# Kernel tuning notes

Hardware: AMD Instinct MI355X
Metric: run time of the kernel (lower is better)

## Reference

```python
import jax, jax.numpy as jnp
import numpy as np

N = 50000   # nodes
E = 400000  # edges (before self-loops)
F = 128     # num_features
H = 8       # heads (layer 1)
C = 64      # hidden_channels
B = 64      # graphs in batch
K = 10      # num_classes
NEG_SLOPE = 0.2


def setup_inputs() -> dict:
    key = jax.random.key(0)
    ks = jax.random.split(key, 12)
    g = lambda k, shape, fan: jax.random.normal(k, shape, jnp.float32) / np.sqrt(fan).astype(np.float32)
    return {
        "x": jax.random.normal(ks[0], (N, F), jnp.float32),
        "edge_index": jax.random.randint(ks[1], (2, E), 0, N, jnp.int32),
        "batch": jnp.sort(jax.random.randint(ks[2], (N,), 0, B, jnp.int32)),
        "W1": g(ks[3], (F, H * C), F),
        "att_src1": g(ks[4], (H, C), C),
        "att_dst1": g(ks[5], (H, C), C),
        "b1": jnp.zeros((H * C,), jnp.float32),
        "W2": g(ks[6], (H * C, C), H * C),
        "att_src2": g(ks[7], (1, C), C),
        "att_dst2": g(ks[8], (1, C), C),
        "b2": jnp.zeros((C,), jnp.float32),
        "lin1_w": g(ks[9], (C, C), C),
        "lin1_b": jnp.zeros((C,), jnp.float32),
        "lin2_w": g(ks[10], (C, K), C),
        "lin2_b": jnp.zeros((K,), jnp.float32),
    }


def gat_conv(x, src, dst, W, att_src, att_dst, bias):
    """PyG GATConv (self-loops already appended to src/dst). x:[N,Fin] -> [N,H*C]."""
    heads, out_c = att_src.shape
    h = (x @ W).reshape(N, heads, out_c)                      # [N,H,C]
    a_s = jnp.einsum('nhc,hc->nh', h, att_src)                # [N,H]
    a_d = jnp.einsum('nhc,hc->nh', h, att_dst)
    e = jax.nn.leaky_relu(a_s[src] + a_d[dst], NEG_SLOPE)     # [E',H]
    # segment softmax over incoming edges of each destination node
    m = jax.ops.segment_max(e, dst, num_segments=N)
    e = jnp.exp(e - m[dst])
    denom = jax.ops.segment_sum(e, dst, num_segments=N)
    alpha = e / (denom[dst] + 1e-16)                          # [E',H]
    out = jax.ops.segment_sum(h[src] * alpha[:, :, None], dst, num_segments=N)  # [N,H,C]
    return out.reshape(N, heads * out_c) + bias


def reference(x, edge_index, batch, W1, att_src1, att_dst1, b1,
              W2, att_src2, att_dst2, b2, lin1_w, lin1_b, lin2_w, lin2_b):
    loops = jnp.arange(N, dtype=edge_index.dtype)
    src = jnp.concatenate([edge_index[0], loops])
    dst = jnp.concatenate([edge_index[1], loops])

    h = gat_conv(x, src, dst, W1, att_src1, att_dst1, b1)     # [N, H*C]
    h = jax.nn.elu(h)                                         # dropout inactive (eval)
    h = gat_conv(h, src, dst, W2, att_src2, att_dst2, b2)     # [N, C]
    h = jax.nn.elu(h)

    pooled = jax.ops.segment_sum(h, batch, num_segments=B)    # global_add_pool -> [B, C]
    z = jax.nn.elu(pooled @ lin1_w + lin1_b)
    logits = z @ lin2_w + lin2_b
    return jax.nn.log_softmax(logits, axis=-1)
```

## Files before the change

kernel.cpp:

```cpp
#include <hip/hip_runtime.h>
#include <hip/hip_bf16.h>

#define DEV static __device__ __forceinline__

constexpr int F1 = 128;
constexpr int H1 = 8;
constexpr int C  = 64;
constexpr int B  = 64;
constexpr int K  = 10;
constexpr float NEG = 0.2f;
constexpr unsigned SMASK = 0x07FFFFFFu;

typedef __attribute__((ext_vector_type(8))) short short8;
typedef __attribute__((ext_vector_type(4))) float floatx4;

DEV float b2f(__hip_bfloat16 x) { return __bfloat162float(x); }
DEV float elu1(float v) { return v > 0.f ? v : (__expf(v) - 1.f); }
DEV unsigned short f2bbits(float f) {
  __hip_bfloat16 b = __float2bfloat16(f);
  return *(unsigned short*)&b;
}
DEV float blo(unsigned u) { return __uint_as_float(u << 16); }
DEV float bhi(unsigned u) { return __uint_as_float(u & 0xffff0000u); }
DEV float bu(unsigned short u) { return __uint_as_float(((unsigned)u) << 16); }
DEV unsigned pack2(float lo, float hi) {
  return (unsigned)f2bbits(lo) | ((unsigned)f2bbits(hi) << 16);
}
DEV float rcp_nr(float x) {
  float r = __builtin_amdgcn_rcpf(x);
  return r * (2.f - x * r);
}


DEV int detect_dev(const void* xraw, int* lds) {
  if (threadIdx.x == 0) {
    const __hip_bfloat16* xb = (const __hip_bfloat16*)xraw;
    int bad = 0;
    for (int i = 0; i < 128; ++i) {
      float v = b2f(xb[2 * i]);
      if (!(fabsf(v) < 1e4f)) bad++;
    }
    *lds = (bad < 13) ? 1 : 0;
  }
  __syncthreads();
  return *lds;
}

#define CVT(p, i) (isbf ? b2f(((const __hip_bfloat16*)(p))[i]) : ((const float*)(p))[i])

__global__ void fused_prep_kernel(const void* x_raw, const void* w1raw,
                                  const void* as1r, const void* ad1r, const void* b1r,
                                  const void* w2raw,
                                  const void* as2r, const void* ad2r, const void* b2r,
                                  const void* l1wr, const void* l1br,
                                  const void* l2wr, const void* l2br,
                                  unsigned short* __restrict__ xbf,
                                  unsigned short* __restrict__ w1frag,
                                  unsigned short* __restrict__ w2frag,
                                  unsigned short* __restrict__ vfrag,
                                  float* __restrict__ wts,
                                  int* __restrict__ deg,
                                  float* __restrict__ pooled,
                                  int nX, int N) {
  __shared__ int fl;
  int isbf = detect_dev(x_raw, &fl);
  int gid = blockIdx.x * 256 + threadIdx.x;
  int stride = gridDim.x * 256;

  int ng = nX >> 3;
  if (isbf) {
    const uint4* src = (const uint4*)x_raw;
    uint4* dst = (uint4*)xbf;
    for (int i = gid; i < ng; i += stride) dst[i] = src[i];
  } else {
    const float4* src = (const float4*)x_raw;
    uint4* dst = (uint4*)xbf;
    for (int i = gid; i < ng; i += stride) {
      float4 a = src[2 * i], b = src[2 * i + 1];
      uint4 o;
      o.x = pack2(a.x, a.y); o.y = pack2(a.z, a.w);
      o.z = pack2(b.x, b.y); o.w = pack2(b.z, b.w);
      dst[i] = o;
    }
  }
  for (int i = ng * 8 + gid; i < nX; i += stride)
    xbf[i] = isbf ? ((const unsigned short*)x_raw)[i]
                  : f2bbits(((const float*)x_raw)[i]);

  for (int i = gid; i < 512;  i += stride) {
    int hp = i >> 7, l16 = (i >> 3) & 15, nt = i & 7;
    int c = hp * 128 + nt * 16 + l16;
    wts[1024 + i] = CVT(b1r, c);
  }
  for (int i = gid; i < 64;   i += stride) wts[1536 + i] = CVT(as2r, i);
  for (int i = gid; i < 64;   i += stride) wts[1600 + i] = CVT(ad2r, i);
  for (int i = gid; i < 64;   i += stride) wts[1664 + i] = CVT(b2r, i);
  for (int i = gid; i < 4096; i += stride) wts[1728 + i] = CVT(l1wr, i);
  for (int i = gid; i < 64;   i += stride) wts[5824 + i] = CVT(l1br, i);
  for (int i = gid; i < 640;  i += stride) wts[5888 + i] = CVT(l2wr, i);
  for (int i = gid; i < 10;   i += stride) wts[6528 + i] = CVT(l2br, i);
  for (int t = gid; t < 8192; t += stride) {
    int lane = t & 63, ks = (t >> 6) & 3, nt = t >> 8;
    for (int j = 0; j < 8; ++j) {
      int k = ks * 32 + (lane >> 4) * 8 + j;
      int n = nt * 16 + (lane & 15);
      w1frag[t * 8 + j] = f2bbits(CVT(w1raw, k * 512 + n));
    }
  }
  for (int t = gid; t < 4096; t += stride) {
    int lane = t & 63, nt = (t >> 6) & 3, ks = t >> 8;
    for (int j = 0; j < 8; ++j) {
      int p = ks * 32 + (lane >> 4) * 8 + j;
      int hp = p >> 7, pl16 = (p >> 3) & 15, pnt = p & 7;
      int k = hp * 128 + pnt * 16 + pl16;
      int n = nt * 16 + (lane & 15);
      w2frag[t * 8 + j] = f2bbits(CVT(w2raw, k * 64 + n));
    }
  }
  for (int t = gid; t < 2048; t += stride) {
    int j = t & 7, lane = (t >> 3) & 63, ks = t >> 9;
    int k = ks * 32 + (lane >> 4) * 8 + j;
    int n = lane & 15;
    int hh = (n < 8) ? n : (n - 8);
    float s = 0.f;
    if (n < 8) {
      for (int c = 0; c < 64; ++c)
        s += CVT(w1raw, k * 512 + hh * 64 + c) * CVT(as1r, hh * 64 + c);
    } else {
      for (int c = 0; c < 64; ++c)
        s += CVT(w1raw, k * 512 + hh * 64 + c) * CVT(ad1r, hh * 64 + c);
    }
    vfrag[(ks * 64 + lane) * 8 + j] = f2bbits(s);
  }
  for (int i = gid; i < N; i += stride) deg[i] = 0;
  for (int i = gid; i < B * C; i += stride) pooled[i] = 0.f;
}

__global__ __launch_bounds__(256) void deg_att_kernel(
    const int* __restrict__ ei, int E, int Etot, int* __restrict__ deg,
    const unsigned short* __restrict__ xbf,
    const unsigned short* __restrict__ vfrag,
    float* __restrict__ a_s, float* __restrict__ a_d,
    int N, int attBlocks) {
  if ((int)blockIdx.x >= attBlocks) {
    int e = ((int)blockIdx.x - attBlocks) * 256 + threadIdx.x;
    if (e < Etot) {
      int d = (e < E) ? ei[E + e] : e - E;
      atomicAdd(&deg[d], 1);
    }
    return;
  }
  int t = threadIdx.x, w = t >> 6, lane = t & 63;
  int quad = lane >> 4, l16 = lane & 15;
  int row0 = blockIdx.x * 64 + w * 16;

  floatx4 acc = {};
  int rl = row0 + l16; if (rl >= N) rl = N - 1;
  const unsigned short* xp = xbf + (size_t)rl * 128 + quad * 8;
#pragma unroll
  for (int ks = 0; ks < 4; ++ks) {
    short8 a = *(const short8*)(xp + ks * 32);
    short8 b = *(const short8*)&vfrag[(ks * 64 + lane) * 8];
    acc = __builtin_amdgcn_mfma_f32_16x16x32_bf16(a, b, acc, 0, 0, 0);
  }
#pragma unroll
  for (int r = 0; r < 4; ++r) {
    int row = row0 + quad * 4 + r;
    if (row < N) {
      if (l16 < 8) a_s[(size_t)row * 8 + l16] = acc[r];
      else         a_d[(size_t)row * 8 + (l16 - 8)] = acc[r];
    }
  }
}

__global__ void scan_block_kernel(const int* __restrict__ deg,
                                  int* __restrict__ local,
                                  int* __restrict__ bsum, int N) {
  __shared__ int tmp[256];
  int t = threadIdx.x;
  int i = blockIdx.x * 256 + t;
  int v = (i < N) ? deg[i] : 0;
  tmp[t] = v;
  __syncthreads();
  for (int off = 1; off < 256; off <<= 1) {
    int u = (t >= off) ? tmp[t - off] : 0;
    __syncthreads();
    tmp[t] += u;
    __syncthreads();
  }
  if (i < N) local[i] = tmp[t] - v;
  if (t == 255) bsum[blockIdx.x] = tmp[255];
}

__global__ void scan_finish_kernel(const int* __restrict__ local,
                                   const int* __restrict__ bsum, int nb,
                                   int* __restrict__ rowptr,
                                   int* __restrict__ cursor, int N, int Etot) {
  __shared__ int tmp[256];
  __shared__ int offs;
  int t = threadIdx.x;
  int v0 = (t < nb) ? bsum[t] : 0;
  tmp[t] = v0;
  __syncthreads();
  for (int off = 1; off < 256; off <<= 1) {
    int u = (t >= off) ? tmp[t - off] : 0;
    __syncthreads();
    tmp[t] += u;
    __syncthreads();
  }
  if (t == (int)blockIdx.x) offs = tmp[t] - v0;
  __syncthreads();
  int i = blockIdx.x * 256 + t;
  if (i < N) {
    int r = local[i] + offs;
    rowptr[i] = r;
    cursor[i] = r;
  }
  if (i == 0) rowptr[N] = Etot;
}

__global__ void fill_weight_kernel(const int* __restrict__ ei, int E, int Etot,
                                   const float* __restrict__ a_s,
                                   const float* __restrict__ a_d,
                                   int* __restrict__ cursor,
                                   int* __restrict__ col,
                                   unsigned short* __restrict__ wedge) {
  int e = blockIdx.x * 256 + threadIdx.x;
  if (e >= Etot) return;
  int s, d;
  if (e < E) { s = ei[e]; d = ei[E + e]; } else { s = d = e - E; }
  int pos = atomicAdd(&cursor[d], 1);
  col[pos] = s | ((d & 15) << 27);
  float4 s0 = *(const float4*)(a_s + (size_t)s * 8);
  float4 s1 = *(const float4*)(a_s + (size_t)s * 8 + 4);
  float4 d0 = *(const float4*)(a_d + (size_t)d * 8);
  float4 d1 = *(const float4*)(a_d + (size_t)d * 8 + 4);
  float v, w0, w1, w2, w3, w4, w5, w6, w7;
  v = s0.x + d0.x; v = v > 0.f ? v : NEG * v; w0 = __expf(v);
  v = s0.y + d0.y; v = v > 0.f ? v : NEG * v; w1 = __expf(v);
  v = s0.z + d0.z; v = v > 0.f ? v : NEG * v; w2 = __expf(v);
  v = s0.w + d0.w; v = v > 0.f ? v : NEG * v; w3 = __expf(v);
  v = s1.x + d1.x; v = v > 0.f ? v : NEG * v; w4 = __expf(v);
  v = s1.y + d1.y; v = v > 0.f ? v : NEG * v; w5 = __expf(v);
  v = s1.z + d1.z; v = v > 0.f ? v : NEG * v; w6 = __expf(v);
  v = s1.w + d1.w; v = v > 0.f ? v : NEG * v; w7 = __expf(v);
  uint4 o;
  o.x = pack2(w0, w1); o.y = pack2(w2, w3);
  o.z = pack2(w4, w5); o.w = pack2(w6, w7);
  *(uint4*)(wedge + (size_t)pos * 8) = o;
}

__global__ __launch_bounds__(512, 6) void aggx_gemm12_kernel(
    const unsigned short* __restrict__ xbf,
    const unsigned short* __restrict__ W1frag,
    const int* __restrict__ rowptr,
    const int* __restrict__ col,
    const unsigned short* __restrict__ wedge,
    const float* __restrict__ bias_perm,
    const unsigned short* __restrict__ W2frag,
    const float* __restrict__ att_src2,
    const float* __restrict__ att_dst2,
    unsigned short* __restrict__ h2,
    float* __restrict__ a_s2, float* __restrict__ a_d2,
    int N) {
  __shared__ __align__(16) char LB[8 * 16 * 136 * 2];

  int t = threadIdx.x, w = t >> 6, lane = t & 63;
  int q = lane >> 4, n = lane & 15;
  int dbase = blockIdx.x * 16;

  int R0 = rowptr[dbase];
  int R1 = rowptr[min(dbase + 16, N)];
  int nch = (R1 - R0 + 31) >> 5;

  int kp = t >> 5, pp = t & 31;
  int skey = (pp & 7) << 4;
  int dw = t >> 5, kw = t & 31;

  short8 onesf = {};
  if (n == 0) {
#pragma unroll
    for (int j = 0; j < 8; ++j) onesf[j] = (short)0x3F80;
  }

  floatx4 accw[8] = {};
  floatx4 accdn = {};

  uint2 pxa, pxb;
  uint4 pwv;
  int pcv;
  {
    int e0 = R0 + 2 * kp;
    int ec0 = min(e0, R1 - 1), ec1 = min(e0 + 1, R1 - 1);
    int s0 = col[ec0] & SMASK;
    int s1 = col[ec1] & SMASK;
    pxa = *(const uint2*)(xbf + (size_t)s0 * 128 + pp * 4);
    pxb = *(const uint2*)(xbf + (size_t)s1 * 128 + pp * 4);
    int ew = min(R0 + kw, R1 - 1);
    pcv = col[ew];
    pwv = *(const uint4*)(wedge + (size_t)ew * 8);
  }

  for (int c = 0; c < nch; ++c) {
    char* Lb = LB + (c & 1) * 16384;
    unsigned short* XgTc = (unsigned short*)Lb;
    unsigned short* Wmc  = (unsigned short*)(Lb + 8192);

    {
      int base = 256 * pp + 4 * kp;
      unsigned w0 = (pxa.x & 0xffffu) | (pxb.x << 16);
      unsigned w1 = (pxa.x >> 16) | (pxb.x & 0xffff0000u);
      unsigned w2 = (pxa.y & 0xffffu) | (pxb.y << 16);
      unsigned w3 = (pxa.y >> 16) | (pxb.y & 0xffff0000u);
      *(unsigned*)(Lb + ((base)       ^ skey)) = w0;
      *(unsigned*)(Lb + ((base + 64)  ^ skey)) = w1;
      *(unsigned*)(Lb + ((base + 128) ^ skey)) = w2;
      *(unsigned*)(Lb + ((base + 192) ^ skey)) = w3;

      int ew = R0 + c * 32 + kw;
      int dl = (pcv >> 27) & 15;
      bool mine = (ew < R1) && (dl == dw);
      unsigned short* wmp = Wmc + dw * 32 + kw;
      wmp[0]    = mine ? (unsigned short)(pwv.x & 0xffff) : 0;
      wmp[512]  = mine ? (unsigned short)(pwv.x >> 16)    : 0;
      wmp[1024] = mine ? (unsigned short)(pwv.y & 0xffff) : 0;
      wmp[1536] = mine ? (unsigned short)(pwv.y >> 16)    : 0;
      wmp[2048] = mine ? (unsigned short)(pwv.z & 0xffff) : 0;
      wmp[2560] = mine ? (unsigned short)(pwv.z >> 16)    : 0;
      wmp[3072] = mine ? (unsigned short)(pwv.w & 0xffff) : 0;
      wmp[3584] = mine ? (unsigned short)(pwv.w >> 16)    : 0;
    }
    if (c + 1 < nch) {
      int ebase = R0 + (c + 1) * 32;
      int e0 = ebase + 2 * kp;
      int ec0 = min(e0, R1 - 1), ec1 = min(e0 + 1, R1 - 1);
      int s0 = col[ec0] & SMASK;
      int s1 = col[ec1] & SMASK;
      pxa = *(const uint2*)(xbf + (size_t)s0 * 128 + pp * 4);
      pxb = *(const uint2*)(xbf + (size_t)s1 * 128 + pp * 4);
      int ew = min(ebase + kw, R1 - 1);
      pcv = col[ew];
      pwv = *(const uint4*)(wedge + (size_t)ew * 8);
    }
    __syncthreads();

    short8 af = *(const short8*)(Wmc + w * 512 + n * 32 + 8 * q);
    accdn = __builtin_amdgcn_mfma_f32_16x16x32_bf16(af, onesf, accdn, 0, 0, 0);
#pragma unroll
    for (int ft = 0; ft < 8; ++ft) {
      int f = ft * 16 + n;
      int bb = f * 64 + 16 * q;
      bb ^= ((f >> 2) & 7) << 4;
      short8 bfr = *(const short8*)((const char*)XgTc + bb);
      accw[ft] = __builtin_amdgcn_mfma_f32_16x16x32_bf16(af, bfr, accw[ft], 0, 0, 0);
    }
  }

  __syncthreads();

  unsigned short* AggP = (unsigned short*)LB;
  {
    float dnv[4];
#pragma unroll
    for (int r = 0; r < 4; ++r) {
      float dr = __shfl(accdn[r], lane & 48);
      dnv[r] = rcp_nr(dr + 1e-16f);
    }
#pragma unroll
    for (int ft = 0; ft < 8; ++ft)
#pragma unroll
      for (int r = 0; r < 4; ++r)
        AggP[w * 2176 + (4 * q + r) * 136 + ft * 16 + n] =
            f2bbits(accw[ft][r] * dnv[r]);
  }
  __syncthreads();

  int hp = w >> 1, qq = w & 1;
  floatx4 acc2[4] = {};
  {
    const unsigned short* Bp = W1frag + (size_t)hp * 16384;
#pragma unroll
    for (int ks = 0; ks < 4; ++ks) {
      short8 a2 = *(const short8*)&AggP[w * 2176 + n * 136 + ks * 32 + q * 8];
#pragma unroll
      for (int j = 0; j < 4; ++j) {
        int nt = qq * 4 + j;
        short8 b2 = *(const short8*)&Bp[((nt * 4 + ks) * 64 + lane) * 8];
        acc2[j] = __builtin_amdgcn_mfma_f32_16x16x32_bf16(a2, b2, acc2[j], 0, 0, 0);
      }
    }
  }
  float4 bq = *(const float4*)&bias_perm[hp * 128 + n * 8 + qq * 4];
  __syncthreads();

  unsigned short* O1 = (unsigned short*)LB;
  float* RED = (float*)(LB + 16640);
  float* PSb = (float*)(LB + 20736);
  float* PDb = (float*)(LB + 20800);

  {
#pragma unroll
    for (int r = 0; r < 4; ++r) {
      int dl = 4 * q + r;
      unsigned short* op = O1 + dl * 520 + hp * 128 + n * 8 + qq * 4;
      op[0] = f2bbits(elu1(acc2[0][r] + bq.x));
      op[1] = f2bbits(elu1(acc2[1][r] + bq.y));
      op[2] = f2bbits(elu1(acc2[2][r] + bq.z));
      op[3] = f2bbits(elu1(acc2[3][r] + bq.w));
    }
    if (t < 32) ((float*)(LB + 20736))[t] = 0.f;
  }
  __syncthreads();

  int nt2 = w & 3, kh = w >> 2;
  floatx4 acc3 = {};
#pragma unroll
  for (int ks8 = 0; ks8 < 8; ++ks8) {
    int ks = kh * 8 + ks8;
    short8 a3 = *(const short8*)&O1[n * 520 + ks * 32 + q * 8];
    short8 b3 = *(const short8*)&W2frag[((ks * 4 + nt2) * 64 + lane) * 8];
    acc3 = __builtin_amdgcn_mfma_f32_16x16x32_bf16(a3, b3, acc3, 0, 0, 0);
  }
  if (kh == 1) *(floatx4*)&RED[(nt2 * 64 + lane) * 4] = acc3;
  __syncthreads();

  if (kh == 0) {
    floatx4 other = *(const floatx4*)&RED[(nt2 * 64 + lane) * 4];
    float asw = att_src2[nt2 * 16 + n];
    float adw = att_dst2[nt2 * 16 + n];
    float ps[4], pd[4];
#pragma unroll
    for (int r = 0; r < 4; ++r) {
      float v = acc3[r] + other[r];
      int row = dbase + 4 * q + r;
      if (row < N) h2[(size_t)row * 64 + nt2 * 16 + n] = f2bbits(v);
      ps[r] = v * asw;
      pd[r] = v * adw;
    }
#pragma unroll
    for (int r = 0; r < 4; ++r) {
      float p = ps[r], qd = pd[r];
#pragma unroll
      for (int off2 = 1; off2 < 16; off2 <<= 1) {
        p += __shfl_xor(p, off2);
        qd += __shfl_xor(qd, off2);
      }
      if (n == 0) {
        int dl = 4 * q + r;
        atomicAdd(&PSb[dl], p);
        atomicAdd(&PDb[dl], qd);
      }
    }
  }
  __syncthreads();
  if (t < 16) {
    int row = dbase + t;
    if (row < N) {
      a_s2[row] = PSb[t];
      a_d2[row] = PDb[t];
    }
  }
}

__global__ void gat_agg1_kernel(const int* __restrict__ rowptr,
                                const int* __restrict__ col,
                                const float* __restrict__ a_s,
                                const float* __restrict__ a_d,
                                const unsigned short* __restrict__ hfeat,
                                const float* __restrict__ bias,
                                unsigned short* __restrict__ out, int N) {
  int wave = threadIdx.x >> 6, lane = threadIdx.x & 63;
  int d = blockIdx.x * 4 + wave;
  if (d >= N) return;
  int beg = rowptr[d], end = rowptr[d + 1];
  int qg = lane >> 4, l16 = lane & 15;
  float adv = a_d[d];
  const uint2* hfu = (const uint2*)hfeat;
  float acc[4] = {};
  float wsum = 0.f;
#pragma unroll 2
  for (int i = beg + qg; i < end; i += 4) {
    int s = col[i] & SMASK;
    float v = a_s[s] + adv;
    v = v > 0.f ? v : NEG * v;
    float wv = __expf(v);
    wsum += wv;
    uint2 u = hfu[(size_t)s * 16 + l16];
    acc[0] += wv * blo(u.x); acc[1] += wv * bhi(u.x);
    acc[2] += wv * blo(u.y); acc[3] += wv * bhi(u.y);
  }
#pragma unroll
  for (int off = 16; off <= 32; off <<= 1) {
#pragma unroll
    for (int j = 0; j < 4; ++j) acc[j] += __shfl_xor(acc[j], off);
    wsum += __shfl_xor(wsum, off);
  }
  float winv = 1.f / (wsum + 1e-16f);
  float4 bb = ((const float4*)bias)[l16];
  float r0 = elu1(acc[0] * winv + bb.x), r1 = elu1(acc[1] * winv + bb.y);
  float r2 = elu1(acc[2] * winv + bb.z), r3 = elu1(acc[3] * winv + bb.w);
  if (qg == 0) {
    uint2 o; o.x = pack2(r0, r1); o.y = pack2(r2, r3);
    ((uint2*)out)[(size_t)d * 16 + l16] = o;
  }
}

__global__ void pool_kernel(const unsigned short* __restrict__ out2,
                            const int* __restrict__ batch,
                            float* __restrict__ pooled, int N) {
  int wave = threadIdx.x >> 6, lane = threadIdx.x & 63;
  int seg = blockIdx.x * 4 + wave;
  int start = seg * 16;
  if (start >= N) return;
  int end = min(start + 16, N);
  int cur = batch[start];
  float acc = 0.f;
  for (int n = start; n < end; ++n) {
    int bn = batch[n];
    if (bn != cur) {
      unsafeAtomicAdd(&pooled[cur * 64 + lane], acc);
      acc = 0.f; cur = bn;
    }
    acc += bu(out2[(size_t)n * 64 + lane]);
  }
  unsafeAtomicAdd(&pooled[cur * 64 + lane], acc);
}

__global__ void head_kernel(const float* __restrict__ pooled,
                            const float* __restrict__ lin1_w,
                            const float* __restrict__ lin1_b,
                            const float* __restrict__ lin2_w,
                            const float* __restrict__ lin2_b,
                            const void* __restrict__ x_raw,
                            void* __restrict__ outv) {
  __shared__ float P[C];
  __shared__ float Zs[C];
  __shared__ float Ls[K];
  __shared__ float lse_s;
  __shared__ int fl;
  int isbf = detect_dev(x_raw, &fl);
  int g = blockIdx.x, t = threadIdx.x;
  P[t] = pooled[g * C + t];
  __syncthreads();
  float acc = lin1_b[t];
  for (int k = 0; k < C; ++k) acc += P[k] * lin1_w[k * C + t];
  Zs[t] = elu1(acc);
  __syncthreads();
  if (t < K) {
    float a = lin2_b[t];
    for (int k = 0; k < C; ++k) a += Zs[k] * lin2_w[k * K + t];
    Ls[t] = a;
  }
  __syncthreads();
  if (t == 0) {
    float mx = -1e30f;
    for (int c = 0; c < K; ++c) mx = fmaxf(mx, Ls[c]);
    float s = 0.f;
    for (int c = 0; c < K; ++c) s += __expf(Ls[c] - mx);
    lse_s = mx + __logf(s);
  }
  __syncthreads();
  if (t < K) {
    float val = Ls[t] - lse_s;
    if (isbf) ((__hip_bfloat16*)outv)[g * K + t] = __float2bfloat16(val);
    else      ((float*)outv)[g * K + t] = val;
  }
}

extern "C" void kernel_launch(void* const* d_in, const int* in_sizes, int n_in,
                              void* d_out, int out_size, void* d_ws, size_t ws_size,
                              hipStream_t stream) {
  const void* x_raw = d_in[0];
  const int*  ei    = (const int*)d_in[1];
  const int*  batch = (const int*)d_in[2];

  const int N    = in_sizes[2];
  const int E    = in_sizes[1] / 2;
  const int Etot = E + N;
  const int nb   = (N + 255) / 256;

  float* ws   = (float*)d_ws;
  size_t off  = 0;

  float* wts = ws + off; off += 6544;
  float* b1w  = wts + 1024;
  float* as2w = wts + 1536;
  float* ad2w = wts + 1600;
  float* b2w  = wts + 1664;
  float* l1w  = wts + 1728;
  float* l1b  = wts + 5824;
  float* l2w  = wts + 5888;
  float* l2b  = wts + 6528;

  unsigned short* xbf    = (unsigned short*)(ws + off); off += (size_t)N * 64;
  unsigned short* w1frag = (unsigned short*)(ws + off); off += 32768;
  unsigned short* w2frag = (unsigned short*)(ws + off); off += 16384;
  unsigned short* vfrag  = (unsigned short*)(ws + off); off += 1024;
  unsigned short* wedge  = (unsigned short*)(ws + off); off += (size_t)Etot * 4;
  unsigned short* h2bf   = (unsigned short*)(ws + off); off += (size_t)N * 32;
  unsigned short* out2bf = (unsigned short*)(ws + off); off += (size_t)N * 32;
  float* as1  = ws + off; off += (size_t)N * H1;
  float* ad1  = ws + off; off += (size_t)N * H1;
  float* as2  = ws + off; off += (size_t)N;
  float* ad2  = ws + off; off += (size_t)N;
  float* pooled = ws + off; off += (size_t)B * C;

  int* ibase  = (int*)(ws + off);
  int* deg    = ibase;                 ibase += N;
  int* cursor = ibase;                 ibase += N;
  int* rowptr = ibase;                 ibase += N + 1;
  int* locals = ibase;                 ibase += N;
  int* bsum   = ibase;                 ibase += 256;
  int* col    = ibase;                 ibase += Etot;

  fused_prep_kernel<<<1024, 256, 0, stream>>>(
      x_raw, d_in[3], d_in[4], d_in[5], d_in[6], d_in[7], d_in[8], d_in[9],
      d_in[10], d_in[11], d_in[12], d_in[13], d_in[14],
      xbf, w1frag, w2frag, vfrag, wts, deg, pooled, in_sizes[0], N);

  {
    int attBlocks = (N + 63) / 64;
    int degBlocks = (Etot + 255) / 256;
    deg_att_kernel<<<attBlocks + degBlocks, 256, 0, stream>>>(
        ei, E, Etot, deg, xbf, vfrag, as1, ad1, N, attBlocks);
  }

  scan_block_kernel<<<nb, 256, 0, stream>>>(deg, locals, bsum, N);
  scan_finish_kernel<<<nb, 256, 0, stream>>>(locals, bsum, nb, rowptr, cursor, N, Etot);

  fill_weight_kernel<<<(Etot + 255) / 256, 256, 0, stream>>>(
      ei, E, Etot, as1, ad1, cursor, col, wedge);

  aggx_gemm12_kernel<<<(N + 15) / 16, 512, 0, stream>>>(
      xbf, w1frag, rowptr, col, wedge, b1w,
      w2frag, as2w, ad2w, h2bf, as2, ad2, N);

  gat_agg1_kernel<<<(N + 3) / 4, 256, 0, stream>>>(rowptr, col, as2, ad2, h2bf, b2w, out2bf, N);

  pool_kernel<<<(N + 63) / 64, 256, 0, stream>>>(out2bf, batch, pooled, N);
  head_kernel<<<B, 64, 0, stream>>>(pooled, l1w, l1b, l2w, l2b, x_raw, (void*)d_out);
}
```

Measured before the change: 274.7 us.

## Fuse layer-2 aggregation with global add pooling via shared memory

Merges the second GAT aggregation kernel with the pooling kernel. Each block handles 16 nodes and stages their ELU outputs (bf16-rounded) in shared memory, then sums them per graph and adds the result to the pooled buffer atomically. This removes the out2 intermediate round trip through global memory and one kernel launch. Each wave now processes four nodes in sequence rather than one, which lowers parallelism per block. The layer-1 output store in the GEMM kernel is also packed into a single uint2 store instead of four scalar stores.

```diff
diff --git a/kernel.cpp b/kernel.cpp
--- a/kernel.cpp
+++ b/kernel.cpp
@@ -402,11 +402,10 @@
 #pragma unroll
     for (int r = 0; r < 4; ++r) {
       int dl = 4 * q + r;
-      unsigned short* op = O1 + dl * 520 + hp * 128 + n * 8 + qq * 4;
-      op[0] = f2bbits(elu1(acc2[0][r] + bq.x));
-      op[1] = f2bbits(elu1(acc2[1][r] + bq.y));
-      op[2] = f2bbits(elu1(acc2[2][r] + bq.z));
-      op[3] = f2bbits(elu1(acc2[3][r] + bq.w));
+      uint2 ov;
+      ov.x = pack2(elu1(acc2[0][r] + bq.x), elu1(acc2[1][r] + bq.y));
+      ov.y = pack2(elu1(acc2[2][r] + bq.z), elu1(acc2[3][r] + bq.w));
+      *(uint2*)(O1 + dl * 520 + hp * 128 + n * 8 + qq * 4) = ov;
     }
     if (t < 32) ((float*)(LB + 20736))[t] = 0.f;
   }
@@ -462,68 +461,74 @@
   }
 }
 
-__global__ void gat_agg1_kernel(const int* __restrict__ rowptr,
-                                const int* __restrict__ col,
-                                const float* __restrict__ a_s,
-                                const float* __restrict__ a_d,
-                                const unsigned short* __restrict__ hfeat,
-                                const float* __restrict__ bias,
-                                unsigned short* __restrict__ out, int N) {
+__global__ __launch_bounds__(256) void gat_agg1_pool_kernel(
+    const int* __restrict__ rowptr,
+    const int* __restrict__ col,
+    const float* __restrict__ a_s,
+    const float* __restrict__ a_d,
+    const unsigned short* __restrict__ hfeat,
+    const float* __restrict__ bias,
+    const int* __restrict__ batch,
+    float* __restrict__ pooled, int N) {
+  __shared__ float S[16][64];
   int wave = threadIdx.x >> 6, lane = threadIdx.x & 63;
-  int d = blockIdx.x * 4 + wave;
-  if (d >= N) return;
-  int beg = rowptr[d], end = rowptr[d + 1];
   int qg = lane >> 4, l16 = lane & 15;
-  float adv = a_d[d];
+  int base = blockIdx.x * 16;
   const uint2* hfu = (const uint2*)hfeat;
-  float acc[4] = {};
-  float wsum = 0.f;
+  float4 bb = ((const float4*)bias)[l16];
+
+  for (int j = 0; j < 4; ++j) {
+    int d = base + wave * 4 + j;
+    if (d < N) {
+      int beg = rowptr[d], end = rowptr[d + 1];
+      float adv = a_d[d];
+      float acc0 = 0.f, acc1 = 0.f, acc2 = 0.f, acc3 = 0.f, wsum = 0.f;
 #pragma unroll 2
-  for (int i = beg + qg; i < end; i += 4) {
-    int s = col[i] & SMASK;
-    float v = a_s[s] + adv;
-    v = v > 0.f ? v : NEG * v;
-    float wv = __expf(v);
-    wsum += wv;
-    uint2 u = hfu[(size_t)s * 16 + l16];
-    acc[0] += wv * blo(u.x); acc[1] += wv * bhi(u.x);
-    acc[2] += wv * blo(u.y); acc[3] += wv * bhi(u.y);
-  }
-#pragma unroll
-  for (int off = 16; off <= 32; off <<= 1) {
-#pragma unroll
-    for (int j = 0; j < 4; ++j) acc[j] += __shfl_xor(acc[j], off);
-    wsum += __shfl_xor(wsum, off);
-  }
-  float winv = 1.f / (wsum + 1e-16f);
-  float4 bb = ((const float4*)bias)[l16];
-  float r0 = elu1(acc[0] * winv + bb.x), r1 = elu1(acc[1] * winv + bb.y);
-  float r2 = elu1(acc[2] * winv + bb.z), r3 = elu1(acc[3] * winv + bb.w);
-  if (qg == 0) {
-    uint2 o; o.x = pack2(r0, r1); o.y = pack2(r2, r3);
-    ((uint2*)out)[(size_t)d * 16 + l16] = o;
-  }
-}
-
-__global__ void pool_kernel(const unsigned short* __restrict__ out2,
-                            const int* __restrict__ batch,
-                            float* __restrict__ pooled, int N) {
-  int wave = threadIdx.x >> 6, lane = threadIdx.x & 63;
-  int seg = blockIdx.x * 4 + wave;
-  int start = seg * 16;
-  if (start >= N) return;
-  int end = min(start + 16, N);
-  int cur = batch[start];
-  float acc = 0.f;
-  for (int n = start; n < end; ++n) {
-    int bn = batch[n];
-    if (bn != cur) {
-      unsafeAtomicAdd(&pooled[cur * 64 + lane], acc);
-      acc = 0.f; cur = bn;
-    }
-    acc += bu(out2[(size_t)n * 64 + lane]);
-  }
-  unsafeAtomicAdd(&pooled[cur * 64 + lane], acc);
+      for (int i = beg + qg; i < end; i += 4) {
+        int s = col[i] & SMASK;
+        float v = a_s[s] + adv;
+        v = v > 0.f ? v : NEG * v;
+        float wv = __expf(v);
+        wsum += wv;
+        uint2 u = hfu[(size_t)s * 16 + l16];
+        acc0 += wv * blo(u.x); acc1 += wv * bhi(u.x);
+        acc2 += wv * blo(u.y); acc3 += wv * bhi(u.y);
+      }
+#pragma unroll
+      for (int off = 16; off <= 32; off <<= 1) {
+        acc0 += __shfl_xor(acc0, off); acc1 += __shfl_xor(acc1, off);
+        acc2 += __shfl_xor(acc2, off); acc3 += __shfl_xor(acc3, off);
+        wsum += __shfl_xor(wsum, off);
+      }
+      float winv = 1.f / (wsum + 1e-16f);
+      if (qg == 0) {
+        int dl = wave * 4 + j;
+        S[dl][4 * l16 + 0] = bu(f2bbits(elu1(acc0 * winv + bb.x)));
+        S[dl][4 * l16 + 1] = bu(f2bbits(elu1(acc1 * winv + bb.y)));
+        S[dl][4 * l16 + 2] = bu(f2bbits(elu1(acc2 * winv + bb.z)));
+        S[dl][4 * l16 + 3] = bu(f2bbits(elu1(acc3 * winv + bb.w)));
+      }
+    }
+  }
+  __syncthreads();
+
+  if (threadIdx.x < 64) {
+    int ch = threadIdx.x;
+    int cnt = min(16, N - base);
+    if (cnt > 0) {
+      int cur = batch[base];
+      float acc = 0.f;
+      for (int nn = 0; nn < cnt; ++nn) {
+        int bn = batch[base + nn];
+        if (bn != cur) {
+          unsafeAtomicAdd(&pooled[cur * 64 + ch], acc);
+          acc = 0.f; cur = bn;
+        }
+        acc += S[nn][ch];
+      }
+      unsafeAtomicAdd(&pooled[cur * 64 + ch], acc);
+    }
+  }
 }
 
 __global__ void head_kernel(const float* __restrict__ pooled,
@@ -598,7 +603,6 @@
   unsigned short* vfrag  = (unsigned short*)(ws + off); off += 1024;
   unsigned short* wedge  = (unsigned short*)(ws + off); off += (size_t)Etot * 4;
   unsigned short* h2bf   = (unsigned short*)(ws + off); off += (size_t)N * 32;
-  unsigned short* out2bf = (unsigned short*)(ws + off); off += (size_t)N * 32;
   float* as1  = ws + off; off += (size_t)N * H1;
   float* ad1  = ws + off; off += (size_t)N * H1;
   float* as2  = ws + off; off += (size_t)N;
@@ -635,8 +639,8 @@
       xbf, w1frag, rowptr, col, wedge, b1w,
       w2frag, as2w, ad2w, h2bf, as2, ad2, N);
 
-  gat_agg1_kernel<<<(N + 3) / 4, 256, 0, stream>>>(rowptr, col, as2, ad2, h2bf, b2w, out2bf, N);
-
-  pool_kernel<<<(N + 63) / 64, 256, 0, stream>>>(out2bf, batch, pooled, N);
+  gat_agg1_pool_kernel<<<(N + 15) / 16, 256, 0, stream>>>(
+      rowptr, col, as2, ad2, h2bf, b2w, batch, pooled, N);
+
   head_kernel<<<B, 64, 0, stream>>>(pooled, l1w, l1b, l2w, l2b, x_raw, (void*)d_out);
 }
```

New measurement: 268.3 us, median of 2. 2.3% less time.
